# Optimization experiments

Measured on AMD Instinct MI355X. Metric: run time of the kernel, lower is better.

Reference implementation:

```python
import jax, jax.numpy as jnp
import numpy as np

H = 512      # hidden_size
NH = 8       # head_size (num heads)
DH = H // NH # att_size per head
FFN = 2048
B, S = 8, 1024
NEG = -1e9
EPS = 1e-5


def _layernorm(x, g, b):
    mu = jnp.mean(x, axis=-1, keepdims=True)
    var = jnp.var(x, axis=-1, keepdims=True)
    return (x - mu) * jax.lax.rsqrt(var + EPS) * g + b


def setup_inputs() -> dict:
    key = jax.random.key(0)
    ks = jax.random.split(key, 16)
    s = 0.02
    return {
        "x": jax.random.normal(ks[0], (B, S, H), jnp.float32),
        "attn_bias": jax.random.normal(ks[1], (B, S, S), jnp.float32),
        "graph_mask": jax.random.randint(ks[2], (B, S, S), 0, 2, jnp.int32),
        "ln1_g": jnp.ones((H,), jnp.float32),
        "ln1_b": jnp.zeros((H,), jnp.float32),
        "Wq": jax.random.normal(ks[3], (H, H), jnp.float32) * s,
        "bq": jnp.zeros((H,), jnp.float32),
        "Wk": jax.random.normal(ks[4], (H, H), jnp.float32) * s,
        "bk": jnp.zeros((H,), jnp.float32),
        "Wv": jax.random.normal(ks[5], (H, H), jnp.float32) * s,
        "bv": jnp.zeros((H,), jnp.float32),
        "Wo": jax.random.normal(ks[6], (H, H), jnp.float32) * s,
        "bo": jnp.zeros((H,), jnp.float32),
        "ln2_g": jnp.ones((H,), jnp.float32),
        "ln2_b": jnp.zeros((H,), jnp.float32),
        "W1": jax.random.normal(ks[7], (H, FFN), jnp.float32) * s,
        "b1": jnp.zeros((FFN,), jnp.float32),
        "W2": jax.random.normal(ks[8], (FFN, H), jnp.float32) * s,
        "b2": jnp.zeros((H,), jnp.float32),
    }


def reference(x, attn_bias, graph_mask, ln1_g, ln1_b, Wq, bq, Wk, bk, Wv, bv,
              Wo, bo, ln2_g, ln2_b, W1, b1, W2, b2):
    b, s, h = x.shape
    # --- self-attention block (eval mode: dropouts are identity) ---
    y = _layernorm(x, ln1_g, ln1_b)
    q = (y @ Wq + bq).reshape(b, s, NH, DH).transpose(0, 2, 1, 3)  # [B,h,S,d]
    k = (y @ Wk + bk).reshape(b, s, NH, DH).transpose(0, 2, 1, 3)
    v = (y @ Wv + bv).reshape(b, s, NH, DH).transpose(0, 2, 1, 3)
    scale = DH ** -0.5
    scores = jnp.einsum('bhqd,bhkd->bhqk', q * scale, k)  # [B,h,S,S]
    mask = (graph_mask == 0)[:, None, :, :]               # [B,1,S,S] broadcast over heads
    bias = jnp.where(mask, NEG, attn_bias[:, None, :, :])
    scores = scores + bias
    scores = jnp.where(mask, NEG, scores)
    p = jax.nn.softmax(scores, axis=-1)
    o = jnp.einsum('bhqk,bhkd->bhqd', p, v)
    o = o.transpose(0, 2, 1, 3).reshape(b, s, h) @ Wo + bo
    x = x + o
    # --- FFN block ---
    y = _layernorm(x, ln2_g, ln2_b)
    y = jax.nn.gelu(y @ W1 + b1, approximate=False) @ W2 + b2
    return x + y
```

## Files before the change

kernel.cpp:

```cpp
#include <hip/hip_runtime.h>
#include <hip/hip_bf16.h>
#include <type_traits>

static constexpr int kS   = 1024;
static constexpr int kH   = 512;
static constexpr int kFFN = 2048;

using bf16 = __hip_bfloat16;
using short8  = __attribute__((ext_vector_type(8))) short;
using float4v = __attribute__((ext_vector_type(4))) float;
#define MFMA16 __builtin_amdgcn_mfma_f32_16x16x32_bf16

__device__ __forceinline__ unsigned short f2bfu(float f){
  unsigned int u = __float_as_uint(f);
  return (unsigned short)((u + 0x7fffu + ((u >> 16) & 1u)) >> 16);
}
__device__ __forceinline__ float bfu2f(unsigned short u){
  return __uint_as_float(((unsigned int)u) << 16);
}
__device__ __forceinline__ unsigned int pack2(float a, float b){
  return (unsigned int)f2bfu(a) | ((unsigned int)f2bfu(b) << 16);
}
__device__ __forceinline__ void async16(const void* g, void* l){
  __builtin_amdgcn_global_load_lds(
    (const __attribute__((address_space(1))) unsigned int*)g,
    (__attribute__((address_space(3))) unsigned int*)l, 16, 0, 0);
}
__device__ __forceinline__ int swz(int col, int row){
  return (col & ~63) | (((((col>>3)&7) ^ (row&7)))<<3) | (col&7);
}

__global__ __launch_bounds__(256) void ln_kernel(const float* __restrict__ x,
    const float* __restrict__ g, const float* __restrict__ bb, bf16* __restrict__ y){
  int wave = threadIdx.x >> 6, lane = threadIdx.x & 63;
  long row = (long)blockIdx.x * 4 + wave;
  const float* xr = x + row * kH + lane*8;
  float4 a = *(const float4*)xr, c = *(const float4*)(xr+4);
  float v[8] = {a.x,a.y,a.z,a.w,c.x,c.y,c.z,c.w};
  float s=0.f, s2=0.f;
#pragma unroll
  for(int i=0;i<8;i++){ s += v[i]; s2 += v[i]*v[i]; }
#pragma unroll
  for(int o=32; o>=1; o>>=1){ s += __shfl_xor(s,o,64); s2 += __shfl_xor(s2,o,64); }
  float mu  = s * (1.f/kH);
  float rs  = rsqrtf(s2*(1.f/kH) - mu*mu + 1e-5f);
  float gv[8], bv[8];
  {
    float4 t0=*(const float4*)(g+lane*8),  t1=*(const float4*)(g+lane*8+4);
    float4 t2=*(const float4*)(bb+lane*8), t3=*(const float4*)(bb+lane*8+4);
    gv[0]=t0.x;gv[1]=t0.y;gv[2]=t0.z;gv[3]=t0.w;gv[4]=t1.x;gv[5]=t1.y;gv[6]=t1.z;gv[7]=t1.w;
    bv[0]=t2.x;bv[1]=t2.y;bv[2]=t2.z;bv[3]=t2.w;bv[4]=t3.x;bv[5]=t3.y;bv[6]=t3.z;bv[7]=t3.w;
  }
  unsigned int ow[4];
#pragma unroll
  for(int i=0;i<4;i++){
    float a0 = (v[2*i]  -mu)*rs*gv[2*i]   + bv[2*i];
    float a1 = (v[2*i+1]-mu)*rs*gv[2*i+1] + bv[2*i+1];
    ow[i] = pack2(a0, a1);
  }
  *reinterpret_cast<uint4*>(y + row*kH + swz(lane*8, (int)row)) = make_uint4(ow[0],ow[1],ow[2],ow[3]);
}

__global__ __launch_bounds__(256) void prep_wt(const float* __restrict__ W,
    bf16* __restrict__ WT, int K, int N){
  __shared__ unsigned short Ts[64*68];
  int tid=threadIdx.x;
  int kb=blockIdx.y*64, nb=blockIdx.x*64;
  {
    int k=tid>>2, nc=(tid&3)*16;
    const float* p = W + (size_t)(kb+k)*N + nb+nc;
#pragma unroll
    for(int i=0;i<16;i+=4){
      float4 f = *(const float4*)(p+i);
      Ts[k*68+nc+i  ]=f2bfu(f.x); Ts[k*68+nc+i+1]=f2bfu(f.y);
      Ts[k*68+nc+i+2]=f2bfu(f.z); Ts[k*68+nc+i+3]=f2bfu(f.w);
    }
  }
  __syncthreads();
  {
    int n=tid>>2, kc=(tid&3)*16;
    unsigned short tmp[16];
#pragma unroll
    for(int i=0;i<16;i++) tmp[i] = Ts[(kc+i)*68 + n];
    int row = nb+n, kg0 = kc>>3;
    bf16* op = WT + (size_t)row*K + kb;
    *(uint4*)(op + (((kg0  ^(row&7)))<<3)) = *(uint4*)&tmp[0];
    *(uint4*)(op + ((((kg0+1)^(row&7)))<<3)) = *(uint4*)&tmp[8];
  }
}

__global__ __launch_bounds__(256) void bias_eff_kernel(
    const int* __restrict__ mask, const float* __restrict__ bias, bf16* __restrict__ be){
  size_t i8 = ((size_t)blockIdx.x*256 + threadIdx.x)*8;
  int4   m0 = *(const int4*)(mask+i8),   m1 = *(const int4*)(mask+i8+4);
  float4 b0 = *(const float4*)(bias+i8), b1 = *(const float4*)(bias+i8+4);
  const unsigned short NEG = f2bfu(-1e9f);
  unsigned short o[8];
  o[0]=m0.x?f2bfu(b0.x):NEG; o[1]=m0.y?f2bfu(b0.y):NEG;
  o[2]=m0.z?f2bfu(b0.z):NEG; o[3]=m0.w?f2bfu(b0.w):NEG;
  o[4]=m1.x?f2bfu(b1.x):NEG; o[5]=m1.y?f2bfu(b1.y):NEG;
  o[6]=m1.z?f2bfu(b1.z):NEG; o[7]=m1.w?f2bfu(b1.w):NEG;
  *(uint4*)((unsigned short*)be + i8) = *(uint4*)o;
}

__global__ __launch_bounds__(256) void transpose_bf16(
    const bf16* __restrict__ v, bf16* __restrict__ vT, int R)
{
  __shared__ unsigned short Ts[64*72];
  int tid=threadIdx.x;
  int rb = blockIdx.y*64, cb = blockIdx.x*64;
  {
    int r=tid>>2, c=(tid&3)*16;
    const bf16* p = v + (size_t)(rb+r)*kH + cb + c;
    *(uint4*)(&Ts[r*72+c])   = *(const uint4*)p;
    *(uint4*)(&Ts[r*72+c+8]) = *(const uint4*)(p+8);
  }
  __syncthreads();
  {
    int c=tid>>2, kb=(tid&3)*16;
    unsigned short tmp[16];
#pragma unroll
    for(int i=0;i<16;i++) tmp[i] = Ts[(kb+i)*72 + c];
    bf16* op = vT + (size_t)(cb+c)*R + rb + kb;
    *(uint4*)(op)   = *(uint4*)(&tmp[0]);
    *(uint4*)(op+8) = *(uint4*)(&tmp[8]);
  }
}

template<int BN, typename OutT, bool SCALE, bool GELU, bool RES, bool CSW>
__global__ __launch_bounds__(BN, 3) void mfma_gemm(
    const bf16* __restrict__ A, const bf16* __restrict__ BT,
    const float* __restrict__ bias, const float* __restrict__ res,
    OutT* __restrict__ C, int M, int N, int K)
{
  constexpr int W = BN/64;
  __shared__ __align__(16) unsigned short As[64*64];
  __shared__ __align__(16) unsigned short Bs[BN*64];
  int tid=threadIdx.x, lane=tid&63, quad=lane>>4, l16=lane&15;
  int w=__builtin_amdgcn_readfirstlane(tid>>6);
  int m0=blockIdx.y*64, n0=blockIdx.x*BN;
  int wn=w*64;
  int lr=lane>>3, lc=lane&7;
  float4v acc[4][4] = {};
  for(int k0=0;k0<K;k0+=64){
    __syncthreads();
#pragma unroll
    for(int i=0;i<8/W;i++){
      int r = (w*(8/W)+i)*8;
      async16(A + (size_t)(m0+r+lr)*K + k0 + lc*8, &As[r*64]);
    }
#pragma unroll
    for(int i=0;i<8;i++){
      int r = (w*8+i)*8;
      async16(BT + (size_t)(n0+r+lr)*K + k0 + lc*8, &Bs[r*64]);
    }
    __syncthreads();
#pragma unroll
    for(int hf=0;hf<2;hf++){
      short8 af[4], bfv[4];
#pragma unroll
      for(int mi=0;mi<4;mi++){
        int row=mi*16+l16;
        af[mi]=*(const short8*)&As[row*64 + (((hf*4+quad)^(row&7))<<3)];
      }
#pragma unroll
      for(int ni=0;ni<4;ni++){
        int n=wn+ni*16+l16;
        bfv[ni]=*(const short8*)&Bs[n*64 + (((hf*4+quad)^(n&7))<<3)];
      }
#pragma unroll
      for(int ni=0;ni<4;ni++)
#pragma unroll
        for(int mi=0;mi<4;mi++)
          acc[mi][ni]=MFMA16(af[mi],bfv[ni],acc[mi][ni],0,0,0);
    }
  }
#pragma unroll
  for(int ni=0;ni<4;ni++){
    int col=n0+wn+ni*16+l16;
    float bc=bias[col];
#pragma unroll
    for(int mi=0;mi<4;mi++){
#pragma unroll
      for(int r=0;r<4;r++){
        int row=m0+mi*16+quad*4+r;
        float v=acc[mi][ni][r]+bc;
        if constexpr(SCALE) v*=0.125f;
        if constexpr(GELU)  v=0.5f*v*(1.f+erff(v*0.70710678118f));
        size_t idx=(size_t)row*N+col;
        if constexpr(RES) v+=res[idx];
        if constexpr(std::is_same<OutT,float>::value) C[idx]=v;
        else {
          size_t ix = CSW ? ((size_t)row*N + swz(col,row)) : idx;
          reinterpret_cast<unsigned short*>(C)[ix]=f2bfu(v);
        }
      }
    }
  }
}

__global__ __launch_bounds__(256,2) void attn_mfma(
    const bf16* __restrict__ q, const bf16* __restrict__ k,
    const bf16* __restrict__ vT, const bf16* __restrict__ be,
    bf16* __restrict__ o)
{
  __shared__ __align__(16) unsigned short Ks[64*64];
  __shared__ __align__(16) unsigned short Vt[64*64];
  __shared__ __align__(16) unsigned short Bt[64*64];
  __shared__ __align__(16) unsigned short Ps[4*16*72];
  int tid=threadIdx.x, lane=tid&63, quad=lane>>4, l16=lane&15;
  int w=__builtin_amdgcn_readfirstlane(tid>>6);
  int q0=blockIdx.x*64, b=blockIdx.y>>3, h=blockIdx.y&7;
  int lr=lane>>3, lc=lane&7;
  const bf16* qp = q + (size_t)(b*kS + q0 + w*16 + l16)*kH + h*64;
  short8 aq0 = *(const short8*)(qp + quad*8);
  short8 aq1 = *(const short8*)(qp + 32 + quad*8);
  float lpart[4]={0.f,0.f,0.f,0.f};
  float4v oacc[4]={};
  int pb = w*16*72;
  int rql = w*16 + quad*4;
  for(int kt=0;kt<16;kt++){
    int kb=kt*64;
    __syncthreads();
#pragma unroll
    for(int i=0;i<2;i++){
      int rr = w*16 + i*8;
      async16(k  + (size_t)(b*kS+kb+rr+lr)*kH + h*64 + ((lc^lr)<<3), &Ks[rr*64]);
      async16(vT + (size_t)(h*64+rr+lr)*8192 + b*kS + kb + ((lc^lr)<<3), &Vt[rr*64]);
      async16(be + (size_t)(b*kS+q0+rr+lr)*kS + kb + ((lc^lr)<<3), &Bt[rr*64]);
    }
    __syncthreads();
    float4v sa[4];
#pragma unroll
    for(int t=0;t<4;t++){
      int krow=t*16+l16, kx=krow&7;
      short8 b0 = *(const short8*)&Ks[krow*64 + ((quad^kx)<<3)];
      short8 b1 = *(const short8*)&Ks[krow*64 + (((4+quad)^kx)<<3)];
      float4v ci;
#pragma unroll
      for(int r=0;r<4;r++){
        int row = rql + r;
        ci[r] = bfu2f(Bt[row*64 + (((t*2+(l16>>3)) ^ (row&7))<<3) + (l16&7)]);
      }
      ci = MFMA16(aq0,b0,ci,0,0,0);
      sa[t]=MFMA16(aq1,b1,ci,0,0,0);
    }
#pragma unroll
    for(int t=0;t<4;t++){
      int kg = t*2 + (l16>>3), j = l16&7;
#pragma unroll
      for(int r=0;r<4;r++){
        float p = __expf(sa[t][r] - 24.f);
        lpart[r] += p;
        int row = quad*4+r;
        Ps[pb + row*72 + ((kg^(row&7))<<3) + j] = f2bfu(p);
      }
    }
    short8 ap0 = *(const short8*)&Ps[pb + l16*72 + ((quad^(l16&7))<<3)];
    short8 ap1 = *(const short8*)&Ps[pb + l16*72 + (((4+quad)^(l16&7))<<3)];
#pragma unroll
    for(int dt=0;dt<4;dt++){
      int vrow=dt*16+l16, vx=vrow&7;
      short8 bv0=*(const short8*)&Vt[vrow*64+((quad^vx)<<3)];
      short8 bv1=*(const short8*)&Vt[vrow*64+(((4+quad)^vx)<<3)];
      oacc[dt]=MFMA16(ap0,bv0,oacc[dt],0,0,0);
      oacc[dt]=MFMA16(ap1,bv1,oacc[dt],0,0,0);
    }
  }
  float inv[4];
#pragma unroll
  for(int r=0;r<4;r++){
    float l = lpart[r];
    l += __shfl_xor(l,1,64); l += __shfl_xor(l,2,64);
    l += __shfl_xor(l,4,64); l += __shfl_xor(l,8,64);
    inv[r] = 1.f/l;
  }
#pragma unroll
  for(int dt=0;dt<4;dt++)
#pragma unroll
    for(int r=0;r<4;r++){
      int row = b*kS + q0 + rql + r;
      int col = h*64 + dt*16 + l16;
      reinterpret_cast<unsigned short*>(o)[(size_t)row*kH + swz(col,row)] =
        f2bfu(oacc[dt][r]*inv[r]);
    }
}

extern "C" void kernel_launch(void* const* d_in, const int* in_sizes, int n_in,
                              void* d_out, int out_size, void* d_ws, size_t ws_size,
                              hipStream_t stream){
  (void)in_sizes; (void)n_in; (void)out_size; (void)ws_size;
  const float* x         = (const float*)d_in[0];
  const float* attn_bias = (const float*)d_in[1];
  const int*   graph_mask= (const int*)  d_in[2];
  const float* ln1_g = (const float*)d_in[3];
  const float* ln1_b = (const float*)d_in[4];
  const float* Wq = (const float*)d_in[5];
  const float* bq = (const float*)d_in[6];
  const float* Wk = (const float*)d_in[7];
  const float* bk = (const float*)d_in[8];
  const float* Wv = (const float*)d_in[9];
  const float* bv = (const float*)d_in[10];
  const float* Wo = (const float*)d_in[11];
  const float* bo = (const float*)d_in[12];
  const float* ln2_g = (const float*)d_in[13];
  const float* ln2_b = (const float*)d_in[14];
  const float* W1 = (const float*)d_in[15];
  const float* b1 = (const float*)d_in[16];
  const float* W2 = (const float*)d_in[17];
  const float* b2 = (const float*)d_in[18];

  char* wsb = (char*)d_ws;
  const size_t SZ = (size_t)8192 * kH * sizeof(bf16);
  bf16* s0 = (bf16*)(wsb);
  bf16* s1 = (bf16*)(wsb + SZ);
  bf16* s2 = (bf16*)(wsb + 2*SZ);
  bf16* s3 = (bf16*)(wsb + 3*SZ);
  float* outf = (float*)d_out;
  bf16* WvT = (bf16*)d_out;
  bf16* WqT = WvT + 262144;
  bf16* WkT = WvT + 524288;
  bf16* beP = (bf16*)d_out;
  bf16* WoT = s3;
  bf16* W1T = s3 + 262144;
  bf16* W2T = s3 + 262144 + 1048576;

  dim3 blk(256);
  prep_wt<<<dim3(8,8),  blk, 0, stream>>>(Wv, WvT, kH, kH);
  prep_wt<<<dim3(8,8),  blk, 0, stream>>>(Wq, WqT, kH, kH);
  prep_wt<<<dim3(8,8),  blk, 0, stream>>>(Wk, WkT, kH, kH);
  ln_kernel<<<dim3(2048), blk, 0, stream>>>(x, ln1_g, ln1_b, s0);
  mfma_gemm<128,bf16,false,false,false,false><<<dim3(4,128), dim3(128), 0, stream>>>(s0, WvT, bv, nullptr, s1, 8192, kH, kH);
  transpose_bf16<<<dim3(8,128), blk, 0, stream>>>(s1, s3, 8192);
  mfma_gemm<128,bf16,true ,false,false,false><<<dim3(4,128), dim3(128), 0, stream>>>(s0, WqT, bq, nullptr, s1, 8192, kH, kH);
  mfma_gemm<128,bf16,false,false,false,false><<<dim3(4,128), dim3(128), 0, stream>>>(s0, WkT, bk, nullptr, s2, 8192, kH, kH);
  bias_eff_kernel<<<dim3(4096), blk, 0, stream>>>(graph_mask, attn_bias, beP);
  attn_mfma<<<dim3(16,64), blk, 0, stream>>>(s1, s2, s3, beP, s0);
  prep_wt<<<dim3(8,8), blk, 0, stream>>>(Wo, WoT, kH, kH);
  mfma_gemm<128,float,false,false,true,false><<<dim3(4,128), dim3(128), 0, stream>>>(s0, WoT, bo, x, outf, 8192, kH, kH);
  ln_kernel<<<dim3(2048), blk, 0, stream>>>(outf, ln2_g, ln2_b, s0);
  prep_wt<<<dim3(32,8), blk, 0, stream>>>(W1, W1T, kH, kFFN);
  prep_wt<<<dim3(8,32), blk, 0, stream>>>(W2, W2T, kFFN, kH);
  for(int c=0;c<2;c++){
    size_t ro = (size_t)c * 4096 * kH;
    mfma_gemm<128,bf16,false,true ,false,true ><<<dim3(16,64), dim3(128), 0, stream>>>(s0 + ro, W1T, b1, nullptr, s1, 4096, kFFN, kH);
    mfma_gemm<64, float,false,false,true ,false><<<dim3(8,64),  dim3(64),  0, stream>>>(s1, W2T, b2, outf + ro, outf + ro, 4096, kH, kFFN);
  }
}
```

Measured before the change: 383.9 us.

## Fuse Q/K/V projections into one GEMM and enlarge GEMM tiles to 128x128

Packs the transposed Wq, Wk and Wv into a single weight matrix with a concatenated bias and runs one 128x128-tile GEMM that routes each column section to the q, k or v buffer, scaling q by 0.125. This replaces three separate projection launches and lets the layernormed input tile be loaded once per block for all three outputs. The GEMM template gains a BM parameter so the Wo and W1 GEMMs also use 128x128 tiles with four waves, raising data reuse per block. The cost is fewer blocks per launch and higher register and LDS use, which may lower occupancy.

Measured after the change: 376.7 us. No clear change (-1.9%).

```diff
diff --git a/kernel.cpp b/kernel.cpp
--- a/kernel.cpp
+++ b/kernel.cpp
@@ -87,6 +87,12 @@
     *(uint4*)(op + (((kg0  ^(row&7)))<<3)) = *(uint4*)&tmp[0];
     *(uint4*)(op + ((((kg0+1)^(row&7)))<<3)) = *(uint4*)&tmp[8];
   }
+}
+
+__global__ __launch_bounds__(256) void concat3(const float* __restrict__ a,
+    const float* __restrict__ b, const float* __restrict__ c, float* __restrict__ o){
+  int i = blockIdx.x*256 + threadIdx.x;
+  if(i < 1536) o[i] = i<512 ? a[i] : (i<1024 ? b[i-512] : c[i-1024]);
 }
 
 __global__ __launch_bounds__(256) void bias_eff_kernel(
@@ -127,31 +133,33 @@
   }
 }
 
-template<int BN, typename OutT, bool SCALE, bool GELU, bool RES, bool CSW>
-__global__ __launch_bounds__(BN, 3) void mfma_gemm(
+template<int BM, int BN, typename OutT, bool SCALE, bool GELU, bool RES, bool CSW>
+__global__ __launch_bounds__((BM/64)*(BN/64)*64, 3) void mfma_gemm(
     const bf16* __restrict__ A, const bf16* __restrict__ BT,
     const float* __restrict__ bias, const float* __restrict__ res,
     OutT* __restrict__ C, int M, int N, int K)
 {
-  constexpr int W = BN/64;
-  __shared__ __align__(16) unsigned short As[64*64];
+  constexpr int W  = (BM/64)*(BN/64);
+  constexpr int NW = BN/64;
+  constexpr int AC = (BM/8)/W, BC = (BN/8)/W;
+  __shared__ __align__(16) unsigned short As[BM*64];
   __shared__ __align__(16) unsigned short Bs[BN*64];
   int tid=threadIdx.x, lane=tid&63, quad=lane>>4, l16=lane&15;
   int w=__builtin_amdgcn_readfirstlane(tid>>6);
-  int m0=blockIdx.y*64, n0=blockIdx.x*BN;
-  int wn=w*64;
+  int wr = w / NW, wc = w % NW;
+  int m0=blockIdx.y*BM, n0=blockIdx.x*BN;
   int lr=lane>>3, lc=lane&7;
   float4v acc[4][4] = {};
   for(int k0=0;k0<K;k0+=64){
     __syncthreads();
 #pragma unroll
-    for(int i=0;i<8/W;i++){
-      int r = (w*(8/W)+i)*8;
+    for(int i=0;i<AC;i++){
+      int r = (w*AC+i)*8;
       async16(A + (size_t)(m0+r+lr)*K + k0 + lc*8, &As[r*64]);
     }
 #pragma unroll
-    for(int i=0;i<8;i++){
-      int r = (w*8+i)*8;
+    for(int i=0;i<BC;i++){
+      int r = (w*BC+i)*8;
       async16(BT + (size_t)(n0+r+lr)*K + k0 + lc*8, &Bs[r*64]);
     }
     __syncthreads();
@@ -160,12 +168,12 @@
       short8 af[4], bfv[4];
 #pragma unroll
       for(int mi=0;mi<4;mi++){
-        int row=mi*16+l16;
+        int row=wr*64+mi*16+l16;
         af[mi]=*(const short8*)&As[row*64 + (((hf*4+quad)^(row&7))<<3)];
       }
 #pragma unroll
       for(int ni=0;ni<4;ni++){
-        int n=wn+ni*16+l16;
+        int n=wc*64+ni*16+l16;
         bfv[ni]=*(const short8*)&Bs[n*64 + (((hf*4+quad)^(n&7))<<3)];
       }
 #pragma unroll
@@ -177,13 +185,13 @@
   }
 #pragma unroll
   for(int ni=0;ni<4;ni++){
-    int col=n0+wn+ni*16+l16;
+    int col=n0+wc*64+ni*16+l16;
     float bc=bias[col];
 #pragma unroll
     for(int mi=0;mi<4;mi++){
 #pragma unroll
       for(int r=0;r<4;r++){
-        int row=m0+mi*16+quad*4+r;
+        int row=m0+wr*64+mi*16+quad*4+r;
         float v=acc[mi][ni][r]+bc;
         if constexpr(SCALE) v*=0.125f;
         if constexpr(GELU)  v=0.5f*v*(1.f+erff(v*0.70710678118f));
@@ -194,6 +202,71 @@
           size_t ix = CSW ? ((size_t)row*N + swz(col,row)) : idx;
           reinterpret_cast<unsigned short*>(C)[ix]=f2bfu(v);
         }
+      }
+    }
+  }
+}
+
+__global__ __launch_bounds__(256, 3) void mfma_gemm_qkv(
+    const bf16* __restrict__ A, const bf16* __restrict__ BT,
+    const float* __restrict__ bias, bf16* __restrict__ qo,
+    bf16* __restrict__ ko, bf16* __restrict__ vo, int M, int N, int K)
+{
+  __shared__ __align__(16) unsigned short As[128*64];
+  __shared__ __align__(16) unsigned short Bs[128*64];
+  int tid=threadIdx.x, lane=tid&63, quad=lane>>4, l16=lane&15;
+  int w=__builtin_amdgcn_readfirstlane(tid>>6);
+  int wr = w >> 1, wc = w & 1;
+  int m0=blockIdx.y*128, n0=blockIdx.x*128;
+  int lr=lane>>3, lc=lane&7;
+  float4v acc[4][4] = {};
+  for(int k0=0;k0<K;k0+=64){
+    __syncthreads();
+#pragma unroll
+    for(int i=0;i<4;i++){
+      int r = (w*4+i)*8;
+      async16(A + (size_t)(m0+r+lr)*K + k0 + lc*8, &As[r*64]);
+    }
+#pragma unroll
+    for(int i=0;i<4;i++){
+      int r = (w*4+i)*8;
+      async16(BT + (size_t)(n0+r+lr)*K + k0 + lc*8, &Bs[r*64]);
+    }
+    __syncthreads();
+#pragma unroll
+    for(int hf=0;hf<2;hf++){
+      short8 af[4], bfv[4];
+#pragma unroll
+      for(int mi=0;mi<4;mi++){
+        int row=wr*64+mi*16+l16;
+        af[mi]=*(const short8*)&As[row*64 + (((hf*4+quad)^(row&7))<<3)];
+      }
+#pragma unroll
+      for(int ni=0;ni<4;ni++){
+        int n=wc*64+ni*16+l16;
+        bfv[ni]=*(const short8*)&Bs[n*64 + (((hf*4+quad)^(n&7))<<3)];
+      }
+#pragma unroll
+      for(int ni=0;ni<4;ni++)
+#pragma unroll
+        for(int mi=0;mi<4;mi++)
+          acc[mi][ni]=MFMA16(af[mi],bfv[ni],acc[mi][ni],0,0,0);
+    }
+  }
+  int sec = __builtin_amdgcn_readfirstlane(n0 >> 9);
+  unsigned short* dst = (unsigned short*)(sec==0 ? qo : (sec==1 ? ko : vo));
+  float scl = (sec==0) ? 0.125f : 1.0f;
+#pragma unroll
+  for(int ni=0;ni<4;ni++){
+    int col=n0+wc*64+ni*16+l16;
+    float bc=bias[col];
+    int cl=col&511;
+#pragma unroll
+    for(int mi=0;mi<4;mi++){
+#pragma unroll
+      for(int r=0;r<4;r++){
+        int row=m0+wr*64+mi*16+quad*4+r;
+        dst[(size_t)row*512+cl]=f2bfu((acc[mi][ni][r]+bc)*scl);
       }
     }
   }
@@ -317,33 +390,32 @@
   bf16* s2 = (bf16*)(wsb + 2*SZ);
   bf16* s3 = (bf16*)(wsb + 3*SZ);
   float* outf = (float*)d_out;
-  bf16* WvT = (bf16*)d_out;
-  bf16* WqT = WvT + 262144;
-  bf16* WkT = WvT + 524288;
-  bf16* beP = (bf16*)d_out;
+  bf16*  WqkvT = (bf16*)d_out;
+  float* bqkv  = (float*)((char*)d_out + (2u<<20));
+  bf16*  vraw  = (bf16*)((char*)d_out + (8u<<20));
+  bf16*  beP   = (bf16*)d_out;
   bf16* WoT = s3;
   bf16* W1T = s3 + 262144;
   bf16* W2T = s3 + 262144 + 1048576;
 
   dim3 blk(256);
-  prep_wt<<<dim3(8,8),  blk, 0, stream>>>(Wv, WvT, kH, kH);
-  prep_wt<<<dim3(8,8),  blk, 0, stream>>>(Wq, WqT, kH, kH);
-  prep_wt<<<dim3(8,8),  blk, 0, stream>>>(Wk, WkT, kH, kH);
+  prep_wt<<<dim3(8,8),  blk, 0, stream>>>(Wq, WqkvT,          kH, kH);
+  prep_wt<<<dim3(8,8),  blk, 0, stream>>>(Wk, WqkvT + 262144, kH, kH);
+  prep_wt<<<dim3(8,8),  blk, 0, stream>>>(Wv, WqkvT + 524288, kH, kH);
+  concat3<<<dim3(6), blk, 0, stream>>>(bq, bk, bv, bqkv);
   ln_kernel<<<dim3(2048), blk, 0, stream>>>(x, ln1_g, ln1_b, s0);
-  mfma_gemm<128,bf16,false,false,false,false><<<dim3(4,128), dim3(128), 0, stream>>>(s0, WvT, bv, nullptr, s1, 8192, kH, kH);
-  transpose_bf16<<<dim3(8,128), blk, 0, stream>>>(s1, s3, 8192);
-  mfma_gemm<128,bf16,true ,false,false,false><<<dim3(4,128), dim3(128), 0, stream>>>(s0, WqT, bq, nullptr, s1, 8192, kH, kH);
-  mfma_gemm<128,bf16,false,false,false,false><<<dim3(4,128), dim3(128), 0, stream>>>(s0, WkT, bk, nullptr, s2, 8192, kH, kH);
+  mfma_gemm_qkv<<<dim3(12,64), blk, 0, stream>>>(s0, WqkvT, bqkv, s1, s2, vraw, 8192, 3*kH, kH);
+  transpose_bf16<<<dim3(8,128), blk, 0, stream>>>(vraw, s3, 8192);
   bias_eff_kernel<<<dim3(4096), blk, 0, stream>>>(graph_mask, attn_bias, beP);
   attn_mfma<<<dim3(16,64), blk, 0, stream>>>(s1, s2, s3, beP, s0);
   prep_wt<<<dim3(8,8), blk, 0, stream>>>(Wo, WoT, kH, kH);
-  mfma_gemm<128,float,false,false,true,false><<<dim3(4,128), dim3(128), 0, stream>>>(s0, WoT, bo, x, outf, 8192, kH, kH);
+  mfma_gemm<128,128,float,false,false,true,false><<<dim3(4,64), blk, 0, stream>>>(s0, WoT, bo, x, outf, 8192, kH, kH);
   ln_kernel<<<dim3(2048), blk, 0, stream>>>(outf, ln2_g, ln2_b, s0);
   prep_wt<<<dim3(32,8), blk, 0, stream>>>(W1, W1T, kH, kFFN);
   prep_wt<<<dim3(8,32), blk, 0, stream>>>(W2, W2T, kFFN, kH);
   for(int c=0;c<2;c++){
     size_t ro = (size_t)c * 4096 * kH;
-    mfma_gemm<128,bf16,false,true ,false,true ><<<dim3(16,64), dim3(128), 0, stream>>>(s0 + ro, W1T, b1, nullptr, s1, 4096, kFFN, kH);
-    mfma_gemm<64, float,false,false,true ,false><<<dim3(8,64),  dim3(64),  0, stream>>>(s1, W2T, b2, outf + ro, outf + ro, 4096, kH, kFFN);
-  }
-}
+    mfma_gemm<128,128,bf16,false,true ,false,true ><<<dim3(16,32), blk, 0, stream>>>(s0 + ro, W1T, b1, nullptr, s1, 4096, kFFN, kH);
+    mfma_gemm<64,64,  float,false,false,true ,false><<<dim3(8,64),  dim3(64), 0, stream>>>(s1, W2T, b2, outf + ro, outf + ro, 4096, kH, kFFN);
+  }
+}
```
